# Kernel optimization log

Measured on AMD Instinct MI355X. Metric: run time of the kernel, lower is better.

## Reference

```python
import jax, jax.numpy as jnp
import numpy as np

V = 25000
E = 100000
NODE_IN = 74
EDGE_IN = 12
OUT = 64
EHID = 128
NUM_STEPS = 6


def setup_inputs() -> dict:
    key = jax.random.key(0)
    ks = jax.random.split(key, 12)
    s = 0.05
    node_feats = jax.random.normal(ks[0], (V, NODE_IN), dtype=jnp.float32)
    edge_feats = jax.random.normal(ks[1], (E, EDGE_IN), dtype=jnp.float32)
    src = jax.random.randint(ks[2], (E,), 0, V)
    dst = jax.random.randint(ks[3], (E,), 0, V)
    # project_node_feats: Linear(node_in, out)
    Wp = jax.random.normal(ks[4], (NODE_IN, OUT), dtype=jnp.float32) * s
    bp = jnp.zeros((OUT,), dtype=jnp.float32)
    # edge network: Linear(edge_in, ehid) -> ReLU -> Linear(ehid, out*out)
    We1 = jax.random.normal(ks[5], (EDGE_IN, EHID), dtype=jnp.float32) * s
    be1 = jnp.zeros((EHID,), dtype=jnp.float32)
    We2 = jax.random.normal(ks[6], (EHID, OUT * OUT), dtype=jnp.float32) * s
    be2 = jnp.zeros((OUT * OUT,), dtype=jnp.float32)
    # NNConv output bias
    bias = jnp.zeros((OUT,), dtype=jnp.float32)
    return {
        "node_feats": node_feats, "edge_feats": edge_feats,
        "src": src, "dst": dst,
        "Wp": Wp, "bp": bp,
        "We1": We1, "be1": be1, "We2": We2, "be2": be2,
        "bias": bias,
    }


def reference(node_feats, edge_feats, src, dst, Wp, bp, We1, be1, We2, be2, bias):
    # project node features
    h = jax.nn.relu(node_feats @ Wp + bp)  # [V, OUT]
    # per-edge weight matrices (same every step -> hoist out of loop)
    ew = jax.nn.relu(edge_feats @ We1 + be1) @ We2 + be2  # [E, OUT*OUT]
    ew = ew.reshape(E, OUT, OUT)
    for _ in range(NUM_STEPS):
        # gather src node feats, batched matvec, scatter-sum to dst
        msg = jnp.einsum('ei,eio->eo', h[src], ew)  # [E, OUT]
        agg = jax.ops.segment_sum(msg, dst, num_segments=V)  # [V, OUT]
        h = jax.nn.relu(agg + bias)
    return h
```

## Files before the change

kernel.cpp:

```cpp
#include <hip/hip_runtime.h>
#include <hip/hip_bf16.h>

#define Vn 25000
#define En 100000
#define NODE_IN 74
#define EDGE_IN 12
#define OUTD 64
#define EHID 128
#define NUM_STEPS 6

#define HPAD 68

typedef __attribute__((ext_vector_type(8))) _Float16 half8;
typedef __attribute__((ext_vector_type(4))) float floatx4;

__global__ void proj_kernel(const float* __restrict__ node,
                            const float* __restrict__ Wp,
                            const float* __restrict__ bp,
                            float* __restrict__ h) {
  __shared__ float nf[NODE_IN];
  int v = blockIdx.x;
  int o = threadIdx.x;
  for (int i = o; i < NODE_IN; i += 64) nf[i] = node[(size_t)v * NODE_IN + i];
  __syncthreads();
  float acc = bp[o];
  for (int i = 0; i < NODE_IN; ++i) acc = fmaf(nf[i], Wp[i * OUTD + o], acc);
  h[(size_t)v * OUTD + o] = fmaxf(acc, 0.0f);
}

__global__ void edge_kernel(const float* __restrict__ ef,
                            const float* __restrict__ We1,
                            const float* __restrict__ be1,
                            _Float16* __restrict__ f) {
  __shared__ float es[EDGE_IN];
  int e = blockIdx.x;
  int k = threadIdx.x;
  if (k < EDGE_IN) es[k] = ef[(size_t)e * EDGE_IN + k];
  __syncthreads();
  float acc = be1[k];
  for (int j = 0; j < EDGE_IN; ++j) acc = fmaf(es[j], We1[j * EHID + k], acc);
  f[(size_t)e * EHID + k] = (_Float16)fmaxf(acc, 0.0f);
}

__global__ void w2r_kernel(const float* __restrict__ We2,
                           _Float16* __restrict__ w2s) {
  int g = blockIdx.x * 256 + threadIdx.x;
  int j = g & 7;
  int quad = (g >> 3) & 3;
  int l15 = (g >> 5) & 15;
  int s = (g >> 9) & 3;
  int wv = (g >> 11) & 3;
  int i = g >> 13;
  int k = s * 32 + quad * 8 + j;
  int col = i * 64 + wv * 16 + l15;
  w2s[g] = (_Float16)We2[(size_t)k * (OUTD * OUTD) + col];
}

__global__ __launch_bounds__(256) void msg_kernel(
    const float* __restrict__ h,
    const _Float16* __restrict__ f,
    const _Float16* __restrict__ w2s,
    const int* __restrict__ src,
    const int* __restrict__ dst,
    const float* __restrict__ be2,
    float* __restrict__ agg) {
  __shared__ float h_t[64 * HPAD];
  __shared__ int s_dst[64];

  const int tid = threadIdx.x;
  const int wv = tid >> 6;
  const int lane = tid & 63;
  const int quad = lane >> 4;
  const int l15 = lane & 15;
  const int e0 = blockIdx.x * 64;

  if (tid < 64) {
    int e = e0 + tid;
    s_dst[tid] = (e < En) ? dst[e] : -1;
  }
  {
    int e = tid & 63;
    int ib = tid >> 6;
    int eg = e0 + e;
    int sv = (eg < En) ? src[eg] : 0;
    const float4* hp = reinterpret_cast<const float4*>(h + (size_t)sv * OUTD + ib * 16);
    for (int c = 0; c < 4; ++c) {
      float4 val = hp[c];
      int i4 = ib * 16 + c * 4;
      h_t[(i4 + 0) * HPAD + e] = val.x;
      h_t[(i4 + 1) * HPAD + e] = val.y;
      h_t[(i4 + 2) * HPAD + e] = val.z;
      h_t[(i4 + 3) * HPAD + e] = val.w;
    }
  }
  __syncthreads();

  half8 afr[4][4];
  for (int t = 0; t < 4; ++t) {
    int e = e0 + t * 16 + l15;
    if (e >= En) e = En - 1;
    const _Float16* fr = f + (size_t)e * EHID + quad * 8;
    for (int s = 0; s < 4; ++s)
      afr[t][s] = *reinterpret_cast<const half8*>(fr + s * 32);
  }

  const _Float16* w2b = w2s + wv * 2048 + l15 * 32 + quad * 8;

#define LOADB(dstv, ii)                                                     \
  {                                                                         \
    const _Float16* p_ = w2b + (size_t)(ii) * 8192;                         \
    dstv[0] = *reinterpret_cast<const half8*>(p_);                          \
    dstv[1] = *reinterpret_cast<const half8*>(p_ + 512);                    \
    dstv[2] = *reinterpret_cast<const half8*>(p_ + 1024);                   \
    dstv[3] = *reinterpret_cast<const half8*>(p_ + 1536);                   \
  }

  floatx4 msgacc[4];
  const floatx4 zero4 = (floatx4){0.f, 0.f, 0.f, 0.f};
  for (int t = 0; t < 4; ++t) msgacc[t] = zero4;

  half8 ba[4], bb[4];
  LOADB(ba, 0);
  LOADB(bb, 1);

#define BODY(iv, breg)                                                         \
  {                                                                            \
    _Float16 hf[4];                                                            \
    for (int t = 0; t < 4; ++t)                                                \
      hf[t] = (_Float16)h_t[(iv) * HPAD + t * 16 + l15];                       \
    half8 hb[4];                                                               \
    for (int t = 0; t < 4; ++t)                                                \
      hb[t] = (half8){hf[t], hf[t], hf[t], hf[t], hf[t], hf[t], hf[t], hf[t]}; \
    for (int s = 0; s < 4; ++s)                                                \
      for (int t = 0; t < 4; ++t) {                                            \
        half8 as = afr[t][s] * hb[t];                                          \
        msgacc[t] = __builtin_amdgcn_mfma_f32_16x16x32_f16(as, breg[s],        \
                                                           msgacc[t], 0, 0, 0); \
      }                                                                        \
  }

  for (int ii = 0; ii < 32; ++ii) {
    int i0 = 2 * ii;
    BODY(i0, ba);
    {
      int inx = (i0 + 2 < 64) ? i0 + 2 : 63;
      LOADB(ba, inx);
    }
    BODY(i0 + 1, bb);
    {
      int inx = (i0 + 3 < 64) ? i0 + 3 : 63;
      LOADB(bb, inx);
    }
  }

  {
    half8 b2f8[2];
    for (int s = 0; s < 2; ++s) {
      half8 v;
      for (int j = 0; j < 8; ++j)
        v[j] = (_Float16)be2[(s * 32 + quad * 8 + j) * 64 + wv * 16 + l15];
      b2f8[s] = v;
    }
    for (int t = 0; t < 4; ++t) {
      half8 ha[2];
      for (int s = 0; s < 2; ++s)
        for (int j = 0; j < 8; ++j)
          ha[s][j] = (_Float16)h_t[(s * 32 + quad * 8 + j) * HPAD + t * 16 + l15];
      msgacc[t] = __builtin_amdgcn_mfma_f32_16x16x32_f16(ha[0], b2f8[0], msgacc[t], 0, 0, 0);
      msgacc[t] = __builtin_amdgcn_mfma_f32_16x16x32_f16(ha[1], b2f8[1], msgacc[t], 0, 0, 0);
    }
  }

  int col = wv * 16 + l15;
  for (int t = 0; t < 4; ++t) {
    int rb = t * 16 + quad * 4;
    for (int r = 0; r < 4; ++r) {
      int d = s_dst[rb + r];
      if (d >= 0) atomicAdd(&agg[(size_t)d * OUTD + col], msgacc[t][r]);
    }
  }
}

__global__ void update_kernel(float* __restrict__ agg,
                              const float* __restrict__ bias,
                              float* __restrict__ hout,
                              float* __restrict__ dout, int last) {
  int g = blockIdx.x * 256 + threadIdx.x;
  if (g >= Vn * OUTD) return;
  float v = agg[g];
  agg[g] = 0.0f;
  float r = fmaxf(v + bias[g & 63], 0.0f);
  hout[g] = r;
  if (last) dout[g] = r;
}

extern "C" void kernel_launch(void* const* d_in, const int* in_sizes, int n_in,
                              void* d_out, int out_size, void* d_ws, size_t ws_size,
                              hipStream_t stream) {
  const float* node = (const float*)d_in[0];
  const float* edge = (const float*)d_in[1];
  const int* src = (const int*)d_in[2];
  const int* dst = (const int*)d_in[3];
  const float* Wp   = (const float*)d_in[4];
  const float* bp   = (const float*)d_in[5];
  const float* We1  = (const float*)d_in[6];
  const float* be1  = (const float*)d_in[7];
  const float* We2  = (const float*)d_in[8];
  const float* be2  = (const float*)d_in[9];
  const float* bias = (const float*)d_in[10];
  float* out = (float*)d_out;

  char* ws = (char*)d_ws;
  float* agg = (float*)(ws);
  float* h_a = (float*)(ws + 6400000);
  float* h_b = (float*)(ws + 12800000);
  _Float16* f   = (_Float16*)(ws + 19200000);
  _Float16* w2s = (_Float16*)(ws + 44800000);

  hipMemsetAsync(agg, 0, (size_t)Vn * OUTD * sizeof(float), stream);
  proj_kernel<<<Vn, 64, 0, stream>>>(node, Wp, bp, h_a);
  edge_kernel<<<En, 128, 0, stream>>>(edge, We1, be1, f);
  w2r_kernel<<<(OUTD * OUTD * EHID) / 256, 256, 0, stream>>>(We2, w2s);

  float* hin = h_a;
  float* hout = h_b;
  for (int s = 0; s < NUM_STEPS; ++s) {
    msg_kernel<<<(En + 63) / 64, 256, 0, stream>>>(hin, f, w2s, src, dst, be2, agg);
    update_kernel<<<(Vn * OUTD + 255) / 256, 256, 0, stream>>>(
        agg, bias, hout, out, s == NUM_STEPS - 1);
    float* t = hin; hin = hout; hout = t;
  }
}
```

Measured before the change: 927.2 us.

## Split msg kernel K-dimension across waves with LDS cross-wave reduction

```diff
diff --git a/kernel.cpp b/kernel.cpp
--- a/kernel.cpp
+++ b/kernel.cpp
@@ -56,7 +56,7 @@
   w2s[g] = (_Float16)We2[(size_t)k * (OUTD * OUTD) + col];
 }
 
-__global__ __launch_bounds__(256) void msg_kernel(
+__global__ __launch_bounds__(256, 2) void msg_kernel(
     const float* __restrict__ h,
     const _Float16* __restrict__ f,
     const _Float16* __restrict__ w2s,
@@ -64,7 +64,7 @@
     const int* __restrict__ dst,
     const float* __restrict__ be2,
     float* __restrict__ agg) {
-  __shared__ float h_t[64 * HPAD];
+  __shared__ __align__(16) float smem[8192];
   __shared__ int s_dst[64];
 
   const int tid = threadIdx.x;
@@ -87,98 +87,137 @@
     for (int c = 0; c < 4; ++c) {
       float4 val = hp[c];
       int i4 = ib * 16 + c * 4;
-      h_t[(i4 + 0) * HPAD + e] = val.x;
-      h_t[(i4 + 1) * HPAD + e] = val.y;
-      h_t[(i4 + 2) * HPAD + e] = val.z;
-      h_t[(i4 + 3) * HPAD + e] = val.w;
+      smem[(i4 + 0) * HPAD + e] = val.x;
+      smem[(i4 + 1) * HPAD + e] = val.y;
+      smem[(i4 + 2) * HPAD + e] = val.z;
+      smem[(i4 + 3) * HPAD + e] = val.w;
     }
   }
   __syncthreads();
 
   half8 afr[4][4];
+#pragma unroll
   for (int t = 0; t < 4; ++t) {
     int e = e0 + t * 16 + l15;
     if (e >= En) e = En - 1;
     const _Float16* fr = f + (size_t)e * EHID + quad * 8;
+#pragma unroll
     for (int s = 0; s < 4; ++s)
       afr[t][s] = *reinterpret_cast<const half8*>(fr + s * 32);
   }
 
-  const _Float16* w2b = w2s + wv * 2048 + l15 * 32 + quad * 8;
-
-#define LOADB(dstv, ii)                                                     \
+  const _Float16* w2l = w2s + l15 * 32 + quad * 8;
+
+#define LOADB4(B, II, SS)                                                   \
   {                                                                         \
-    const _Float16* p_ = w2b + (size_t)(ii) * 8192;                         \
-    dstv[0] = *reinterpret_cast<const half8*>(p_);                          \
-    dstv[1] = *reinterpret_cast<const half8*>(p_ + 512);                    \
-    dstv[2] = *reinterpret_cast<const half8*>(p_ + 1024);                   \
-    dstv[3] = *reinterpret_cast<const half8*>(p_ + 1536);                   \
-  }
-
-  floatx4 msgacc[4];
+    const _Float16* p_ = w2l + (size_t)(II) * 8192 + (SS) * 512;            \
+    B[0] = *reinterpret_cast<const half8*>(p_);                             \
+    B[1] = *reinterpret_cast<const half8*>(p_ + 2048);                      \
+    B[2] = *reinterpret_cast<const half8*>(p_ + 4096);                      \
+    B[3] = *reinterpret_cast<const half8*>(p_ + 6144);                      \
+  }
+
+  floatx4 acc[4][4];
   const floatx4 zero4 = (floatx4){0.f, 0.f, 0.f, 0.f};
-  for (int t = 0; t < 4; ++t) msgacc[t] = zero4;
-
-  half8 ba[4], bb[4];
-  LOADB(ba, 0);
-  LOADB(bb, 1);
-
-#define BODY(iv, breg)                                                         \
-  {                                                                            \
-    _Float16 hf[4];                                                            \
-    for (int t = 0; t < 4; ++t)                                                \
-      hf[t] = (_Float16)h_t[(iv) * HPAD + t * 16 + l15];                       \
-    half8 hb[4];                                                               \
-    for (int t = 0; t < 4; ++t)                                                \
-      hb[t] = (half8){hf[t], hf[t], hf[t], hf[t], hf[t], hf[t], hf[t], hf[t]}; \
-    for (int s = 0; s < 4; ++s)                                                \
-      for (int t = 0; t < 4; ++t) {                                            \
-        half8 as = afr[t][s] * hb[t];                                          \
-        msgacc[t] = __builtin_amdgcn_mfma_f32_16x16x32_f16(as, breg[s],        \
-                                                           msgacc[t], 0, 0, 0); \
-      }                                                                        \
-  }
-
-  for (int ii = 0; ii < 32; ++ii) {
-    int i0 = 2 * ii;
-    BODY(i0, ba);
-    {
-      int inx = (i0 + 2 < 64) ? i0 + 2 : 63;
-      LOADB(ba, inx);
+#pragma unroll
+  for (int t = 0; t < 4; ++t)
+#pragma unroll
+    for (int c = 0; c < 4; ++c) acc[t][c] = zero4;
+
+  half8 b0[4], b1[4];
+  const int ibase = wv * 16;
+  LOADB4(b0, ibase, 0);
+
+#define SSTEP(SS, CURB, NXTB, NI, NS)                                         \
+  {                                                                           \
+    LOADB4(NXTB, NI, NS);                                                     \
+    _Pragma("unroll") for (int t = 0; t < 4; ++t) {                           \
+      half8 as = afr[t][SS] * hb[t];                                          \
+      acc[t][0] = __builtin_amdgcn_mfma_f32_16x16x32_f16(as, CURB[0], acc[t][0], 0, 0, 0); \
+      acc[t][1] = __builtin_amdgcn_mfma_f32_16x16x32_f16(as, CURB[1], acc[t][1], 0, 0, 0); \
+      acc[t][2] = __builtin_amdgcn_mfma_f32_16x16x32_f16(as, CURB[2], acc[t][2], 0, 0, 0); \
+      acc[t][3] = __builtin_amdgcn_mfma_f32_16x16x32_f16(as, CURB[3], acc[t][3], 0, 0, 0); \
+    }                                                                         \
+  }
+
+  for (int ii = 0; ii < 16; ++ii) {
+    int iv = ibase + ii;
+    half8 hb[4];
+#pragma unroll
+    for (int t = 0; t < 4; ++t) {
+      _Float16 hf = (_Float16)smem[iv * HPAD + t * 16 + l15];
+      hb[t] = (half8){hf, hf, hf, hf, hf, hf, hf, hf};
     }
-    BODY(i0 + 1, bb);
-    {
-      int inx = (i0 + 3 < 64) ? i0 + 3 : 63;
-      LOADB(bb, inx);
+    int nxi = (ii == 15) ? iv : iv + 1;
+    SSTEP(0, b0, b1, iv, 1);
+    SSTEP(1, b1, b0, iv, 2);
+    SSTEP(2, b0, b1, iv, 3);
+    SSTEP(3, b1, b0, nxi, 0);
+  }
+
+  if (wv == 0) {
+#pragma unroll
+    for (int s = 0; s < 2; ++s) {
+      half8 b2f[4];
+#pragma unroll
+      for (int c = 0; c < 4; ++c) {
+        half8 v;
+#pragma unroll
+        for (int j = 0; j < 8; ++j)
+          v[j] = (_Float16)be2[(s * 32 + quad * 8 + j) * 64 + c * 16 + l15];
+        b2f[c] = v;
+      }
+#pragma unroll
+      for (int t = 0; t < 4; ++t) {
+        half8 ha;
+#pragma unroll
+        for (int j = 0; j < 8; ++j)
+          ha[j] = (_Float16)smem[(s * 32 + quad * 8 + j) * HPAD + t * 16 + l15];
+#pragma unroll
+        for (int c = 0; c < 4; ++c)
+          acc[t][c] = __builtin_amdgcn_mfma_f32_16x16x32_f16(ha, b2f[c], acc[t][c], 0, 0, 0);
+      }
     }
   }
 
-  {
-    half8 b2f8[2];
-    for (int s = 0; s < 2; ++s) {
-      half8 v;
-      for (int j = 0; j < 8; ++j)
-        v[j] = (_Float16)be2[(s * 32 + quad * 8 + j) * 64 + wv * 16 + l15];
-      b2f8[s] = v;
-    }
-    for (int t = 0; t < 4; ++t) {
-      half8 ha[2];
-      for (int s = 0; s < 2; ++s)
-        for (int j = 0; j < 8; ++j)
-          ha[s][j] = (_Float16)h_t[(s * 32 + quad * 8 + j) * HPAD + t * 16 + l15];
-      msgacc[t] = __builtin_amdgcn_mfma_f32_16x16x32_f16(ha[0], b2f8[0], msgacc[t], 0, 0, 0);
-      msgacc[t] = __builtin_amdgcn_mfma_f32_16x16x32_f16(ha[1], b2f8[1], msgacc[t], 0, 0, 0);
-    }
-  }
-
-  int col = wv * 16 + l15;
-  for (int t = 0; t < 4; ++t) {
-    int rb = t * 16 + quad * 4;
-    for (int r = 0; r < 4; ++r) {
-      int d = s_dst[rb + r];
-      if (d >= 0) atomicAdd(&agg[(size_t)d * OUTD + col], msgacc[t][r]);
-    }
-  }
+  floatx4* scv = reinterpret_cast<floatx4*>(smem);
+
+#define ST1(TG)                                                           \
+  _Pragma("unroll") for (int c = 0; c < 4; ++c)                           \
+      scv[wv * 512 + (((TG) & 1) * 4 + c) * 64 + lane] = acc[TG][c];
+#define LD1(TK)                                                           \
+  _Pragma("unroll") for (int c = 0; c < 4; ++c)                           \
+      acc[TK][c] += scv[(wv ^ 1) * 512 + (((TK) & 1) * 4 + c) * 64 + lane];
+#define ST2(TG)                                                           \
+  _Pragma("unroll") for (int c = 0; c < 4; ++c)                           \
+      scv[wv * 512 + c * 64 + lane] = acc[TG][c];
+#define LD2(TK)                                                           \
+  _Pragma("unroll") for (int c = 0; c < 4; ++c)                           \
+      acc[TK][c] += scv[(wv ^ 2) * 512 + c * 64 + lane];
+#define SCAT(TF)                                                          \
+  {                                                                       \
+    int rb = (TF) * 16 + quad * 4;                                        \
+    _Pragma("unroll") for (int c = 0; c < 4; ++c) {                       \
+      int col = c * 16 + l15;                                             \
+      _Pragma("unroll") for (int r = 0; r < 4; ++r) {                     \
+        int d = s_dst[rb + r];                                            \
+        if (d >= 0) atomicAdd(&agg[(size_t)d * OUTD + col], acc[TF][c][r]); \
+      }                                                                   \
+    }                                                                     \
+  }
+
+  __syncthreads();
+  if ((wv & 1) == 0) { ST1(2); ST1(3); } else { ST1(0); ST1(1); }
+  __syncthreads();
+  if ((wv & 1) == 0) { LD1(0); LD1(1); } else { LD1(2); LD1(3); }
+  __syncthreads();
+  if (wv == 0) { ST2(1); } else if (wv == 1) { ST2(3); }
+  else if (wv == 2) { ST2(0); } else { ST2(2); }
+  __syncthreads();
+  if (wv == 0) { LD2(0); SCAT(0); }
+  else if (wv == 1) { LD2(2); SCAT(2); }
+  else if (wv == 2) { LD2(1); SCAT(1); }
+  else { LD2(3); SCAT(3); }
 }
 
 __global__ void update_kernel(float* __restrict__ agg,
```

After: 998.4 us. 1.08x slower.
